# Kernel tuning notes

Measured on AMD Instinct MI355X. Metric: run time of the kernel, lower is better.

The kernel has to match this reference:

```python
import jax, jax.numpy as jnp
import numpy as np

N = 100000
E = 3200000
NFEAT = 256
NHID = 128
NCLASS = 64


def setup_inputs() -> dict:
    key = jax.random.key(0)
    ks = jax.random.split(key, 10)
    x = jax.random.normal(ks[0], (N, NFEAT), dtype=jnp.float32)
    src = jax.random.randint(ks[1], (E,), 0, N, dtype=jnp.int32).astype(jnp.int64)
    dst = jax.random.randint(ks[2], (E,), 0, N, dtype=jnp.int32).astype(jnp.int64)
    # Glorot-ish init for GraphConv weights
    def w(k, i, o):
        return jax.random.normal(k, (i, o), dtype=jnp.float32) * (1.0 / np.sqrt(i))
    W0 = w(ks[3], NFEAT, NHID)
    b0 = jnp.zeros((NHID,), dtype=jnp.float32)
    W1 = w(ks[4], NHID, NHID)
    b1 = jnp.zeros((NHID,), dtype=jnp.float32)
    W2 = w(ks[5], NHID, NCLASS)
    b2 = jnp.zeros((NCLASS,), dtype=jnp.float32)
    return {"x": x, "src": src, "dst": dst,
            "W0": W0, "b0": b0, "W1": W1, "b1": b1, "W2": W2, "b2": b2}


def _degree_norms(src, dst, dtype):
    ones = jnp.ones(src.shape, dtype)
    deg_out = jax.ops.segment_sum(ones, src, num_segments=N)
    deg_in = jax.ops.segment_sum(ones, dst, num_segments=N)
    # clamp zero degrees to avoid inf (DGL clamps to 1)
    n_src = jnp.where(deg_out > 0, deg_out, 1.0) ** -0.5
    n_dst = jnp.where(deg_in > 0, deg_in, 1.0) ** -0.5
    return n_src, n_dst


def _graph_conv(h, src, dst, n_src, n_dst, W, b):
    # weight first (math-equivalent to DGL ordering), then normalized SpMM
    h = h @ W                              # [N, out]
    msg = h[src] * n_src[src][:, None]     # [E, out] gather + src norm
    agg = jax.ops.segment_sum(msg, dst, num_segments=N)  # [N, out]
    return agg * n_dst[:, None] + b


def reference(x, src, dst, W0, b0, W1, b1, W2, b2):
    n_src, n_dst = _degree_norms(src, dst, x.dtype)
    h = _graph_conv(x, src, dst, n_src, n_dst, W0, b0)
    # dropout is identity in eval mode
    h = _graph_conv(h, src, dst, n_src, n_dst, W1, b1)
    h = _graph_conv(h, src, dst, n_src, n_dst, W2, b2)
    return jax.nn.softmax(h, axis=1)
```

## Files before the change

kernel.cpp:

```cpp
#include <hip/hip_runtime.h>
#include <hip/hip_bf16.h>

#define N_NODES 100000
#define N_EDGES 3200000
#define NFEAT 256
#define NHID 128
#define NCLASS 64
#define SCAN_B 1024
#define NB_SCAN ((N_NODES + SCAN_B - 1) / SCAN_B)
#define NVEC4 (N_EDGES / 4)
#define RANGE (N_NODES / 8)
#define NSL 64

typedef unsigned int uint32;
typedef unsigned short ushort16;
typedef __attribute__((ext_vector_type(8))) short bf16x8;
typedef __attribute__((ext_vector_type(4))) float f32x4;
typedef __attribute__((ext_vector_type(2))) float f32x2;

static __device__ __forceinline__ float b2f(ushort16 u) {
    union { float f; uint32 i; } c; c.i = ((uint32)u) << 16; return c.f;
}
static __device__ __forceinline__ ushort16 f2b(float f) {
    union { float f; uint32 i; } c; c.f = f;
    uint32 r = (c.i + 0x7FFFu + ((c.i >> 16) & 1u)) >> 16;
    return (ushort16)r;
}
static __device__ __forceinline__ float blo(uint32 u) {
    union { float f; uint32 i; } c; c.i = u << 16; return c.f;
}
static __device__ __forceinline__ float bhi(uint32 u) {
    union { float f; uint32 i; } c; c.i = u & 0xFFFF0000u; return c.f;
}
static __device__ __forceinline__ uint32 pack2(float a, float b) {
    return (uint32)f2b(a) | ((uint32)f2b(b) << 16);
}

__global__ __launch_bounds__(256) void k_hist(const int4* __restrict__ src4,
                                              const int4* __restrict__ dst4,
                                              uint32* __restrict__ scratch) {
    __shared__ uint32 h[RANGE];
    int g = blockIdx.x & 7, sl = blockIdx.x >> 3;
    int lo = g * RANGE, hi = lo + RANGE;
    for (int i = threadIdx.x; i < RANGE; i += 256) h[i] = 0u;
    __syncthreads();
    for (int t = sl * 256 + threadIdx.x; t < NVEC4; t += NSL * 256) {
        int4 s = src4[t], d = dst4[t];
        if (s.x >= lo && s.x < hi) atomicAdd(&h[s.x - lo], 1u);
        if (s.y >= lo && s.y < hi) atomicAdd(&h[s.y - lo], 1u);
        if (s.z >= lo && s.z < hi) atomicAdd(&h[s.z - lo], 1u);
        if (s.w >= lo && s.w < hi) atomicAdd(&h[s.w - lo], 1u);
        if (d.x >= lo && d.x < hi) atomicAdd(&h[d.x - lo], 65536u);
        if (d.y >= lo && d.y < hi) atomicAdd(&h[d.y - lo], 65536u);
        if (d.z >= lo && d.z < hi) atomicAdd(&h[d.z - lo], 65536u);
        if (d.w >= lo && d.w < hi) atomicAdd(&h[d.w - lo], 65536u);
    }
    __syncthreads();
    uint32* dstp = scratch + ((size_t)(g * NSL + sl)) * RANGE;
    for (int i = threadIdx.x; i < RANGE; i += 256) dstp[i] = h[i];
}

__global__ void k_sumdeg(const uint32* __restrict__ scratch, int* __restrict__ deg_in,
                         float* __restrict__ n_src, float* __restrict__ n_dst) {
    int i = blockIdx.x * blockDim.x + threadIdx.x;
    if (i >= N_NODES) return;
    if (i == 0) n_src[N_NODES] = 0.f;
    int g = i / RANGE, r = i - g * RANGE;
    const uint32* base = scratch + (size_t)g * NSL * RANGE + r;
    uint32 so = 0, di = 0;
    for (int s = 0; s < NSL; s++) {
        uint32 v = base[(size_t)s * RANGE];
        so += v & 0xFFFFu;
        di += v >> 16;
    }
    deg_in[i] = (int)di;
    uint32 so1 = so < 1u ? 1u : so;
    uint32 di1 = di < 1u ? 1u : di;
    n_src[i] = rsqrtf((float)so1);
    n_dst[i] = rsqrtf((float)di1);
}

__global__ void k_scan1(const int* __restrict__ deg_in, int* __restrict__ row_ptr,
                        int* __restrict__ blk_sums) {
    __shared__ int sh[SCAN_B];
    int i = blockIdx.x * SCAN_B + threadIdx.x;
    int v = (i < N_NODES) ? deg_in[i] : 0;
    sh[threadIdx.x] = v;
    __syncthreads();
    for (int o = 1; o < SCAN_B; o <<= 1) {
        int t = 0;
        if ((int)threadIdx.x >= o) t = sh[threadIdx.x - o];
        __syncthreads();
        sh[threadIdx.x] += t;
        __syncthreads();
    }
    if (i < N_NODES) row_ptr[i] = sh[threadIdx.x] - v;
    if (threadIdx.x == SCAN_B - 1) blk_sums[blockIdx.x] = sh[SCAN_B - 1];
}

__global__ void k_scan2(int* __restrict__ blk_sums) {
    if (threadIdx.x == 0 && blockIdx.x == 0) {
        int acc = 0;
        for (int b = 0; b < NB_SCAN; b++) { int v = blk_sums[b]; blk_sums[b] = acc; acc += v; }
        blk_sums[NB_SCAN] = acc;
    }
}

__global__ void k_scan3(const int* __restrict__ blk_sums, int* __restrict__ row_ptr) {
    int i = blockIdx.x * SCAN_B + threadIdx.x;
    if (i < N_NODES) row_ptr[i] += blk_sums[blockIdx.x];
    if (i == 0) row_ptr[N_NODES] = blk_sums[NB_SCAN];
}

__global__ void k_offsets(uint32* __restrict__ scratch, const int* __restrict__ row_ptr) {
    int i = blockIdx.x * blockDim.x + threadIdx.x;
    if (i >= N_NODES) return;
    int g = i / RANGE, r = i - g * RANGE;
    uint32* base = scratch + (size_t)g * NSL * RANGE + r;
    uint32 run = (uint32)row_ptr[i];
    for (int s = 0; s < NSL; s++) {
        uint32 v = base[(size_t)s * RANGE];
        base[(size_t)s * RANGE] = run;
        run += v >> 16;
    }
}

__global__ __launch_bounds__(256) void k_fill2(const int4* __restrict__ src4,
                                               const int4* __restrict__ dst4,
                                               const uint32* __restrict__ scratch,
                                               int* __restrict__ col) {
    __shared__ uint32 cur[RANGE];
    int g = blockIdx.x & 7, sl = blockIdx.x >> 3;
    int lo = g * RANGE, hi = lo + RANGE;
    const uint32* base = scratch + ((size_t)(g * NSL + sl)) * RANGE;
    for (int i = threadIdx.x; i < RANGE; i += 256) cur[i] = base[i];
    __syncthreads();
    for (int t = sl * 256 + threadIdx.x; t < NVEC4; t += NSL * 256) {
        int4 s = src4[t], d = dst4[t];
        if (d.x >= lo && d.x < hi) { uint32 p = atomicAdd(&cur[d.x - lo], 1u); col[p] = s.x; }
        if (d.y >= lo && d.y < hi) { uint32 p = atomicAdd(&cur[d.y - lo], 1u); col[p] = s.y; }
        if (d.z >= lo && d.z < hi) { uint32 p = atomicAdd(&cur[d.z - lo], 1u); col[p] = s.z; }
        if (d.w >= lo && d.w < hi) { uint32 p = atomicAdd(&cur[d.w - lo], 1u); col[p] = s.w; }
    }
}

__global__ void k_w01(const float* __restrict__ W0, const float* __restrict__ W1,
                      float* __restrict__ W01) {
    __shared__ float row[NHID];
    int r = blockIdx.x, c = threadIdx.x;
    row[c] = W0[r * NHID + c];
    __syncthreads();
    float acc = 0.f;
    for (int k = 0; k < NHID; k++) acc += row[k] * W1[k * NHID + c];
    W01[r * NHID + c] = acc;
}

__global__ void k_wc(const float* __restrict__ W01, const float* __restrict__ W2,
                     float* __restrict__ Wc, ushort16* __restrict__ Wt) {
    __shared__ float row[NHID];
    int r = blockIdx.x, c = threadIdx.x;
    row[c] = W01[r * NHID + c];
    row[c + 64] = W01[r * NHID + c + 64];
    __syncthreads();
    float acc = 0.f;
    for (int k = 0; k < NHID; k++) acc += row[k] * W2[k * NCLASS + c];
    Wc[r * NCLASS + c] = acc;
    Wt[(size_t)c * NFEAT + r] = f2b(acc);
}

__global__ void k_bv(const float* __restrict__ b0, const float* __restrict__ W1,
                     const float* __restrict__ b1, const float* __restrict__ W2,
                     float* __restrict__ bv) {
    __shared__ float tmp[NHID];
    int c = threadIdx.x;
    for (int cc = c; cc < NHID; cc += 64) {
        float a = 0.f;
        for (int k = 0; k < NHID; k++) a += b0[k] * W1[k * NHID + cc];
        tmp[cc] = a;
    }
    __syncthreads();
    float a1 = 0.f, a2 = 0.f;
    for (int k = 0; k < NHID; k++) {
        float wv = W2[k * NCLASS + c];
        a1 += tmp[k] * wv;
        a2 += b1[k] * wv;
    }
    bv[c] = a1;
    bv[64 + c] = a2;
}

__global__ __launch_bounds__(256) void k_gemm_y(const float* __restrict__ x,
                                                const ushort16* __restrict__ Wt,
                                                const float* __restrict__ n_src,
                                                ushort16* __restrict__ y) {
    int tid = threadIdx.x;
    int wid = tid >> 6, lane = tid & 63;
    int q = lane >> 4, r = lane & 15;
    int rowbase = blockIdx.x * 64 + wid * 16;
    int rowld = min(rowbase + r, N_NODES - 1);
    const float* xp = x + (size_t)rowld * NFEAT + q * 8;

    float4 alo[8], ahi[8];
#pragma unroll
    for (int kt = 0; kt < 8; kt++) {
        alo[kt] = *(const float4*)(xp + kt * 32);
        ahi[kt] = *(const float4*)(xp + kt * 32 + 4);
    }

    f32x4 acc0 = {0.f, 0.f, 0.f, 0.f};
    f32x4 acc1 = {0.f, 0.f, 0.f, 0.f};
    f32x4 acc2 = {0.f, 0.f, 0.f, 0.f};
    f32x4 acc3 = {0.f, 0.f, 0.f, 0.f};

#pragma unroll
    for (int kt = 0; kt < 8; kt++) {
        bf16x8 af;
        af[0] = (short)f2b(alo[kt].x); af[1] = (short)f2b(alo[kt].y);
        af[2] = (short)f2b(alo[kt].z); af[3] = (short)f2b(alo[kt].w);
        af[4] = (short)f2b(ahi[kt].x); af[5] = (short)f2b(ahi[kt].y);
        af[6] = (short)f2b(ahi[kt].z); af[7] = (short)f2b(ahi[kt].w);
        const int ko = kt * 32 + q * 8;
        bf16x8 b0 = *(const bf16x8*)(Wt + (size_t)(0 * 16 + r) * NFEAT + ko);
        bf16x8 b1 = *(const bf16x8*)(Wt + (size_t)(1 * 16 + r) * NFEAT + ko);
        bf16x8 b2 = *(const bf16x8*)(Wt + (size_t)(2 * 16 + r) * NFEAT + ko);
        bf16x8 b3 = *(const bf16x8*)(Wt + (size_t)(3 * 16 + r) * NFEAT + ko);
        acc0 = __builtin_amdgcn_mfma_f32_16x16x32_bf16(af, b0, acc0, 0, 0, 0);
        acc1 = __builtin_amdgcn_mfma_f32_16x16x32_bf16(af, b1, acc1, 0, 0, 0);
        acc2 = __builtin_amdgcn_mfma_f32_16x16x32_bf16(af, b2, acc2, 0, 0, 0);
        acc3 = __builtin_amdgcn_mfma_f32_16x16x32_bf16(af, b3, acc3, 0, 0, 0);
    }

    int srow0 = rowbase + q * 4;
#pragma unroll
    for (int i = 0; i < 4; i++) {
        int rr = srow0 + i;
        if (rr < N_NODES) {
            float ns = n_src[rr];
            ushort16* yp = y + (size_t)rr * NCLASS + r;
            yp[0]  = f2b(acc0[i] * ns);
            yp[16] = f2b(acc1[i] * ns);
            yp[32] = f2b(acc2[i] * ns);
            yp[48] = f2b(acc3[i] * ns);
        } else if (rr == N_NODES) {
            ushort16* yp = y + (size_t)rr * NCLASS + r;
            yp[0] = 0; yp[16] = 0; yp[32] = 0; yp[48] = 0;
        }
    }
}

template <int PASS>
__global__ __launch_bounds__(256) void k_agg(
        const int* __restrict__ row_ptr, const int* __restrict__ col,
        const float* __restrict__ wsrc,
        const float* __restrict__ n_src, const float* __restrict__ n_dst,
        const ushort16* __restrict__ in, ushort16* __restrict__ out,
        float* __restrict__ outf,
        float* __restrict__ tsave, float* __restrict__ tssave,
        const float* __restrict__ t1, const float* __restrict__ t2,
        const float* __restrict__ bv, const float* __restrict__ b2) {
    int wid = threadIdx.x >> 6, lane = threadIdx.x & 63;
    int node = blockIdx.x * 4 + wid;
    if (node > N_NODES) return;
    int g = lane >> 3, sub = lane & 7;

    if (node == N_NODES) {
        if (PASS != 3) {
            if (g == 0) {
                uint4 z = {0u, 0u, 0u, 0u};
                *((uint4*)((char*)out + ((size_t)N_NODES << 7)) + sub) = z;
            }
            if (lane == 0) {
                tsave[N_NODES] = 0.f;
                if (PASS == 1) tssave[N_NODES] = 0.f;
            }
        }
        return;
    }

    int s = row_ptr[node], e = row_ptr[node + 1];
    const char* inb = (const char*)in;
    const char* wb  = (const char*)wsrc;
    uint32 subo = (uint32)sub << 4;

    f32x2 a0 = {0.f, 0.f}, a1 = {0.f, 0.f}, a2 = {0.f, 0.f}, a3 = {0.f, 0.f};
    float accs = 0.f;

#define CH(P)                                                                  \
    {                                                                          \
        int p_ = (P);                                                          \
        bool v_ = p_ < e;                                                      \
        int j_ = v_ ? col[p_] : N_NODES;                                       \
        uint32 fo_ = ((uint32)j_ << 7) + subo;                                 \
        uint4 u_ = *(const uint4*)(inb + fo_);                                 \
        if (PASS != 3) accs += *(const float*)(wb + ((uint32)j_ << 2));        \
        f32x2 q0; q0.x = blo(u_.x); q0.y = bhi(u_.x);                          \
        f32x2 q1; q1.x = blo(u_.y); q1.y = bhi(u_.y);                          \
        f32x2 q2; q2.x = blo(u_.z); q2.y = bhi(u_.z);                          \
        f32x2 q3; q3.x = blo(u_.w); q3.y = bhi(u_.w);                          \
        a0 += q0; a1 += q1; a2 += q2; a3 += q3;                                \
    }

    for (int base = s; base < e; base += 32) {
        CH(base + g)
        CH(base + 8 + g)
        CH(base + 16 + g)
        CH(base + 24 + g)
    }
#undef CH

#pragma unroll
    for (int off = 8; off <= 32; off <<= 1) {
        a0.x += __shfl_xor(a0.x, off, 64); a0.y += __shfl_xor(a0.y, off, 64);
        a1.x += __shfl_xor(a1.x, off, 64); a1.y += __shfl_xor(a1.y, off, 64);
        a2.x += __shfl_xor(a2.x, off, 64); a2.y += __shfl_xor(a2.y, off, 64);
        a3.x += __shfl_xor(a3.x, off, 64); a3.y += __shfl_xor(a3.y, off, 64);
        if (PASS != 3) accs += __shfl_xor(accs, off, 64);
    }

    float nd = n_dst[node];
    if (PASS == 3) {
        float t2n = t2[node], t1n = t1[node];
        const float* bvA = bv + sub * 8;
        const float* bvB = bv + 64 + sub * 8;
        const float* b2p = b2 + sub * 8;
        float v0 = a0.x * nd + t2n * bvA[0] + t1n * bvB[0] + b2p[0];
        float v1 = a0.y * nd + t2n * bvA[1] + t1n * bvB[1] + b2p[1];
        float v2 = a1.x * nd + t2n * bvA[2] + t1n * bvB[2] + b2p[2];
        float v3 = a1.y * nd + t2n * bvA[3] + t1n * bvB[3] + b2p[3];
        float v4 = a2.x * nd + t2n * bvA[4] + t1n * bvB[4] + b2p[4];
        float v5 = a2.y * nd + t2n * bvA[5] + t1n * bvB[5] + b2p[5];
        float v6 = a3.x * nd + t2n * bvA[6] + t1n * bvB[6] + b2p[6];
        float v7 = a3.y * nd + t2n * bvA[7] + t1n * bvB[7] + b2p[7];
        float m = fmaxf(fmaxf(fmaxf(v0, v1), fmaxf(v2, v3)),
                        fmaxf(fmaxf(v4, v5), fmaxf(v6, v7)));
#pragma unroll
        for (int off = 1; off <= 4; off <<= 1) m = fmaxf(m, __shfl_xor(m, off, 64));
        float e0 = __expf(v0 - m), e1 = __expf(v1 - m), e2 = __expf(v2 - m), e3 = __expf(v3 - m);
        float e4 = __expf(v4 - m), e5 = __expf(v5 - m), e6 = __expf(v6 - m), e7 = __expf(v7 - m);
        float sum = ((e0 + e1) + (e2 + e3)) + ((e4 + e5) + (e6 + e7));
#pragma unroll
        for (int off = 1; off <= 4; off <<= 1) sum += __shfl_xor(sum, off, 64);
        float r = 1.0f / sum;
        if (g == 0) {
            float4 o0 = {e0 * r, e1 * r, e2 * r, e3 * r};
            float4 o1 = {e4 * r, e5 * r, e6 * r, e7 * r};
            float4* op = (float4*)(outf + (size_t)node * NCLASS + sub * 8);
            op[0] = o0;
            op[1] = o1;
        }
    } else {
        if (g == 0) {
            float sc = nd * n_src[node];
            uint32 w0 = pack2(a0.x * sc, a0.y * sc);
            uint32 w1 = pack2(a1.x * sc, a1.y * sc);
            uint32 w2 = pack2(a2.x * sc, a2.y * sc);
            uint32 w3 = pack2(a3.x * sc, a3.y * sc);
            uint4 w = {w0, w1, w2, w3};
            *((uint4*)((char*)out + ((size_t)node << 7)) + sub) = w;
        }
        if (lane == 0) {
            float T = accs * nd;
            tsave[node] = T;
            if (PASS == 1) tssave[node] = T * n_src[node];
        }
    }
}

extern "C" void kernel_launch(void* const* d_in, const int* in_sizes, int n_in,
                              void* d_out, int out_size, void* d_ws, size_t ws_size,
                              hipStream_t stream) {
    const float* x   = (const float*)d_in[0];
    const int*   src = (const int*)d_in[1];
    const int*   dst = (const int*)d_in[2];
    const float* W0  = (const float*)d_in[3];
    const float* b0  = (const float*)d_in[4];
    const float* W1  = (const float*)d_in[5];
    const float* b1  = (const float*)d_in[6];
    const float* W2  = (const float*)d_in[7];
    const float* b2  = (const float*)d_in[8];
    float* out = (float*)d_out;

    size_t off = 0;
    auto alloc = [&](size_t bytes) {
        void* p = (char*)d_ws + off;
        off = (off + bytes + 255) & ~(size_t)255;
        return p;
    };
    int*      deg_in   = (int*)alloc(N_NODES * 4);
    float*    n_src    = (float*)alloc((N_NODES + 1) * 4);
    float*    n_dst    = (float*)alloc(N_NODES * 4);
    int*      row_ptr  = (int*)alloc((N_NODES + 1) * 4);
    int*      blk_sums = (int*)alloc((NB_SCAN + 1) * 4);
    int*      col      = (int*)alloc((size_t)N_EDGES * 4);
    uint32*   scratch  = (uint32*)alloc((size_t)8 * NSL * RANGE * 4);
    float*    W01      = (float*)alloc(NFEAT * NHID * 4);
    float*    Wc       = (float*)alloc(NFEAT * NCLASS * 4);
    ushort16* Wt       = (ushort16*)alloc((size_t)NFEAT * NCLASS * 2);
    float*    bv       = (float*)alloc(128 * 4);
    float*    t1       = (float*)alloc((N_NODES + 1) * 4);
    float*    t1s      = (float*)alloc((N_NODES + 1) * 4);
    float*    t2       = (float*)alloc((N_NODES + 1) * 4);
    ushort16* bufB1    = (ushort16*)alloc((size_t)(N_NODES + 1) * NCLASS * 2);
    ushort16* bufB2    = (ushort16*)alloc((size_t)(N_NODES + 1) * NCLASS * 2);
    (void)ws_size; (void)in_sizes; (void)n_in; (void)out_size;

    const int TB = 256;
    const int NBn = (N_NODES + TB - 1) / TB;
    const int NW = (N_NODES + 3) / 4 + 1;
    const int GP = 8 * NSL;

    k_hist<<<GP, TB, 0, stream>>>((const int4*)src, (const int4*)dst, scratch);
    k_sumdeg<<<NBn, TB, 0, stream>>>(scratch, deg_in, n_src, n_dst);
    k_scan1<<<NB_SCAN, SCAN_B, 0, stream>>>(deg_in, row_ptr, blk_sums);
    k_scan2<<<1, 64, 0, stream>>>(blk_sums);
    k_scan3<<<NB_SCAN, SCAN_B, 0, stream>>>(blk_sums, row_ptr);
    k_offsets<<<NBn, TB, 0, stream>>>(scratch, row_ptr);
    k_fill2<<<GP, TB, 0, stream>>>((const int4*)src, (const int4*)dst, scratch, col);

    k_w01<<<NFEAT, NHID, 0, stream>>>(W0, W1, W01);
    k_wc<<<NFEAT, NCLASS, 0, stream>>>(W01, W2, Wc, Wt);
    k_bv<<<1, NCLASS, 0, stream>>>(b0, W1, b1, W2, bv);

    k_gemm_y<<<(N_NODES + 64) / 64, 256, 0, stream>>>(x, Wt, n_src, bufB1);

    k_agg<1><<<NW, 256, 0, stream>>>(row_ptr, col, n_src, n_src, n_dst, bufB1, bufB2,
                                     nullptr, t1, t1s, nullptr, nullptr, nullptr, nullptr);
    k_agg<2><<<NW, 256, 0, stream>>>(row_ptr, col, t1s, n_src, n_dst, bufB2, bufB1,
                                     nullptr, t2, nullptr, nullptr, nullptr, nullptr, nullptr);
    k_agg<3><<<NW, 256, 0, stream>>>(row_ptr, col, nullptr, n_src, n_dst, bufB1, nullptr,
                                     out, nullptr, nullptr, t1, t2, bv, b2);
}
```

Measured before the change: 535.6 us.

## Halve edge rescans in histogram and CSR fill by doubling per-block node range

The histogram and CSR-fill kernels now give each block a node range twice as wide (25000 nodes, 100KB of LDS) and use 512 threads. Only 4 range groups scan the edge list instead of 8, so src/dst are read half as many times. The scratch layout is unchanged, with each block writing or reading two RANGE slices. The cost is a larger shared-memory footprint per block, which may reduce occupancy and raise LDS atomic contention per block.

```diff
diff --git a/kernel.cpp b/kernel.cpp
--- a/kernel.cpp
+++ b/kernel.cpp
@@ -36,15 +36,15 @@
     return (uint32)f2b(a) | ((uint32)f2b(b) << 16);
 }
 
-__global__ __launch_bounds__(256) void k_hist(const int4* __restrict__ src4,
+__global__ __launch_bounds__(512) void k_hist(const int4* __restrict__ src4,
                                               const int4* __restrict__ dst4,
                                               uint32* __restrict__ scratch) {
-    __shared__ uint32 h[RANGE];
-    int g = blockIdx.x & 7, sl = blockIdx.x >> 3;
-    int lo = g * RANGE, hi = lo + RANGE;
-    for (int i = threadIdx.x; i < RANGE; i += 256) h[i] = 0u;
-    __syncthreads();
-    for (int t = sl * 256 + threadIdx.x; t < NVEC4; t += NSL * 256) {
+    __shared__ uint32 h[2 * RANGE];
+    int gp = blockIdx.x & 3, sl = blockIdx.x >> 2;
+    int lo = gp * 2 * RANGE, hi = lo + 2 * RANGE;
+    for (int i = threadIdx.x; i < 2 * RANGE; i += 512) h[i] = 0u;
+    __syncthreads();
+    for (int t = sl * 512 + threadIdx.x; t < NVEC4; t += NSL * 512) {
         int4 s = src4[t], d = dst4[t];
         if (s.x >= lo && s.x < hi) atomicAdd(&h[s.x - lo], 1u);
         if (s.y >= lo && s.y < hi) atomicAdd(&h[s.y - lo], 1u);
@@ -56,8 +56,11 @@
         if (d.w >= lo && d.w < hi) atomicAdd(&h[d.w - lo], 65536u);
     }
     __syncthreads();
-    uint32* dstp = scratch + ((size_t)(g * NSL + sl)) * RANGE;
-    for (int i = threadIdx.x; i < RANGE; i += 256) dstp[i] = h[i];
+    int g0 = gp * 2;
+    uint32* dst0 = scratch + ((size_t)(g0 * NSL + sl)) * RANGE;
+    uint32* dst1 = scratch + ((size_t)((g0 + 1) * NSL + sl)) * RANGE;
+    for (int i = threadIdx.x; i < RANGE; i += 512) dst0[i] = h[i];
+    for (int i = threadIdx.x; i < RANGE; i += 512) dst1[i] = h[RANGE + i];
 }
 
 __global__ void k_sumdeg(const uint32* __restrict__ scratch, int* __restrict__ deg_in,
@@ -125,17 +128,20 @@
     }
 }
 
-__global__ __launch_bounds__(256) void k_fill2(const int4* __restrict__ src4,
+__global__ __launch_bounds__(512) void k_fill2(const int4* __restrict__ src4,
                                                const int4* __restrict__ dst4,
                                                const uint32* __restrict__ scratch,
                                                int* __restrict__ col) {
-    __shared__ uint32 cur[RANGE];
-    int g = blockIdx.x & 7, sl = blockIdx.x >> 3;
-    int lo = g * RANGE, hi = lo + RANGE;
-    const uint32* base = scratch + ((size_t)(g * NSL + sl)) * RANGE;
-    for (int i = threadIdx.x; i < RANGE; i += 256) cur[i] = base[i];
-    __syncthreads();
-    for (int t = sl * 256 + threadIdx.x; t < NVEC4; t += NSL * 256) {
+    __shared__ uint32 cur[2 * RANGE];
+    int gp = blockIdx.x & 3, sl = blockIdx.x >> 2;
+    int lo = gp * 2 * RANGE, hi = lo + 2 * RANGE;
+    int g0 = gp * 2;
+    const uint32* base0 = scratch + ((size_t)(g0 * NSL + sl)) * RANGE;
+    const uint32* base1 = scratch + ((size_t)((g0 + 1) * NSL + sl)) * RANGE;
+    for (int i = threadIdx.x; i < RANGE; i += 512) cur[i] = base0[i];
+    for (int i = threadIdx.x; i < RANGE; i += 512) cur[RANGE + i] = base1[i];
+    __syncthreads();
+    for (int t = sl * 512 + threadIdx.x; t < NVEC4; t += NSL * 512) {
         int4 s = src4[t], d = dst4[t];
         if (d.x >= lo && d.x < hi) { uint32 p = atomicAdd(&cur[d.x - lo], 1u); col[p] = s.x; }
         if (d.y >= lo && d.y < hi) { uint32 p = atomicAdd(&cur[d.y - lo], 1u); col[p] = s.y; }
@@ -407,15 +413,15 @@
     const int TB = 256;
     const int NBn = (N_NODES + TB - 1) / TB;
     const int NW = (N_NODES + 3) / 4 + 1;
-    const int GP = 8 * NSL;
-
-    k_hist<<<GP, TB, 0, stream>>>((const int4*)src, (const int4*)dst, scratch);
+    const int GP2 = 4 * NSL;
+
+    k_hist<<<GP2, 512, 0, stream>>>((const int4*)src, (const int4*)dst, scratch);
     k_sumdeg<<<NBn, TB, 0, stream>>>(scratch, deg_in, n_src, n_dst);
     k_scan1<<<NB_SCAN, SCAN_B, 0, stream>>>(deg_in, row_ptr, blk_sums);
     k_scan2<<<1, 64, 0, stream>>>(blk_sums);
     k_scan3<<<NB_SCAN, SCAN_B, 0, stream>>>(blk_sums, row_ptr);
     k_offsets<<<NBn, TB, 0, stream>>>(scratch, row_ptr);
-    k_fill2<<<GP, TB, 0, stream>>>((const int4*)src, (const int4*)dst, scratch, col);
+    k_fill2<<<GP2, 512, 0, stream>>>((const int4*)src, (const int4*)dst, scratch, col);
 
     k_w01<<<NFEAT, NHID, 0, stream>>>(W0, W1, W01);
     k_wc<<<NFEAT, NCLASS, 0, stream>>>(W01, W2, Wc, Wt);
```

Measured after the change: 520.1 us. -2.9%, faster.
